# Kernel optimization log

Hardware: AMD Instinct MI355X
Metric: run time of the kernel (lower is better)

## Reference

```python
import jax, jax.numpy as jnp
import numpy as np

B, S1, S2, C = 8, 256, 256, 64
M1, M2 = 32, 32          # n_modes per spatial dim
SCALE = 1.0 / (C * C)    # 1/(in_channels*out_channels)


def setup_inputs() -> dict:
    key = jax.random.key(0)
    ks = jax.random.split(key, 5)
    X = jax.random.normal(ks[0], (B, S1, S2, C), dtype=jnp.float32)
    k0r = SCALE * jax.random.normal(ks[1], (M1, C, C), dtype=jnp.float32)
    k0i = SCALE * jax.random.normal(ks[2], (M1, C, C), dtype=jnp.float32)
    k1r = SCALE * jax.random.normal(ks[3], (M2, C, C), dtype=jnp.float32)
    k1i = SCALE * jax.random.normal(ks[4], (M2, C, C), dtype=jnp.float32)
    return {"X": X, "k0r": k0r, "k0i": k0i, "k1r": k1r, "k1i": k1i}


def reference(X, k0r, k0i, k1r, k1i):
    # Factorized spectral conv: per-spatial-dim rFFT -> truncated-mode
    # complex channel mix -> zero-pad -> irFFT, summed over dims.
    k0 = jax.lax.complex(k0r, k0i)  # (M1, out, in)
    k1 = jax.lax.complex(k1r, k1i)  # (M2, out, in)

    out = jnp.zeros_like(X)

    # --- spatial dim 0 (axis -3) ---
    Xf = jnp.fft.rfft(X, axis=-3, norm="forward")          # (B, S1//2+1, S2, C) complex
    Yt = jnp.einsum("rij,bryj->bryi", k0, Xf[:, :M1])       # truncated-mode channel mix
    Y = jnp.zeros_like(Xf).at[:, :M1].set(Yt)               # zero-pad back to full modes
    out = out + jnp.fft.irfft(Y, n=S1, axis=-3, norm="forward")

    # --- spatial dim 1 (axis -2) ---
    Xf = jnp.fft.rfft(X, axis=-2, norm="forward")           # (B, S1, S2//2+1, C)
    Yt = jnp.einsum("rij,bxrj->bxri", k1, Xf[:, :, :M2])
    Y = jnp.zeros_like(Xf).at[:, :, :M2].set(Yt)
    out = out + jnp.fft.irfft(Y, n=S2, axis=-2, norm="forward")

    return out
```

## Files before the change

kernel.cpp:

```cpp
#include <hip/hip_runtime.h>


namespace {

constexpr int S = 256, C = 64;

typedef _Float16 f16;
typedef _Float16 f16x2 __attribute__((ext_vector_type(2)));
typedef _Float16 f16x4 __attribute__((ext_vector_type(4)));
typedef _Float16 f16x8 __attribute__((ext_vector_type(8)));
typedef float f32x16 __attribute__((ext_vector_type(16)));
typedef unsigned int u32;

constexpr int OFF_FWDF = 0;
constexpr int OFF_INVF = 8192;
constexpr int OFF_A2   = 16384;
constexpr int OFF_YT   = 540672;
constexpr int OFF_XF   = 8929280;
constexpr size_t WS_RMW = (size_t)(OFF_XF + 8388608) * 4;
constexpr size_t WS_PW  = (size_t)(OFF_XF + 16777216) * 4;

constexpr size_t XF_DB = 1048576;
constexpr size_t YT_DB = 1048576;

constexpr int P   = 4624;
constexpr int LDS_BYTES = 8 * P;

__device__ __host__ inline int cadr(int c) { return c * 16 + (c >> 3) * 16; }
__device__ inline int yadr(int r, int c) { return 1152 * r + c * 4 + (c >> 5) * 16; }

__global__ void k_init_all(const float* __restrict__ k0r, const float* __restrict__ k0i,
                           const float* __restrict__ k1r, const float* __restrict__ ki1,
                           float* __restrict__ ws) {
  const int bid = blockIdx.x;
  if (bid < 128) {
    int t = bid * 256 + threadIdx.x;
    f16* fwdF = (f16*)(ws + OFF_FWDF);
    f16* invF = (f16*)(ws + OFF_INVF);
    if (t < 16384) {
      int e = t & 7, lane = (t >> 3) & 63, mtkk = t >> 9;
      int mt = mtkk & 1, kk = mtkk >> 1;
      int mc = mt * 32 + (lane & 31);
      int x = kk * 16 + 8 * (lane >> 5) + e;
      int r = mc >> 1;
      float ang = (float)((r * x) & 255) * (3.14159265358979323846f / 128.0f);
      float v = (mc & 1) ? -sinf(ang) : cosf(ang);
      fwdF[t] = (f16)v;
    } else {
      int t2 = t - 16384;
      int e = t2 & 7, lane = (t2 >> 3) & 63, mtg = (t2 >> 9) & 7, kk = t2 >> 12;
      int u = mtg * 32 + (lane & 31);
      int mcv = kk * 16 + 8 * (lane >> 5) + e;
      int r = mcv >> 1;
      float wgt = (r == 0) ? 1.0f : 2.0f;
      float ang = (float)((r * u) & 255) * (3.14159265358979323846f / 128.0f);
      float v = (mcv & 1) ? -wgt * sinf(ang) : wgt * cosf(ang);
      invF[t2] = (f16)(v * (1.0f / 256.0f));
    }
    return;
  }
  const int db = bid - 128;
  const float* kr = (db < 2048) ? k0r : k1r;
  const float* ki = (db < 2048) ? k0i : ki1;
  f16* A2 = (f16*)(ws + OFF_A2) + ((db < 2048) ? 0 : 524288);
  int t = (db & 2047) * 256 + threadIdx.x;
  int e = t & 7, l = (t >> 3) & 63, kk = (t >> 9) & 7, mt = (t >> 12) & 3, r = t >> 14;
  int m = mt * 32 + (l & 31);
  int kreal = kk * 16 + 8 * (l >> 5) + e;
  int i = m >> 1, imo = m & 1, j = kreal >> 1, imi = kreal & 1;
  int src = (r * 64 + i) * 64 + j;
  float v = (imi == 0) ? ((imo == 0) ? kr[src] : ki[src])
                       : ((imo == 0) ? -ki[src] : kr[src]);
  A2[t] = (f16)v;
}

__launch_bounds__(512, 2)
__global__ void k_dft(const float* __restrict__ X, const float* __restrict__ ws,
                      f16* __restrict__ xfg) {
  __shared__ char sm[LDS_BYTES] __attribute__((aligned(16)));
  const int tid = threadIdx.x;
  const int l = tid & 63, w = tid >> 6;
  const int g2 = l >> 5, l31 = l & 31;
  const int n0 = w * 32;
  const int dim = (int)blockIdx.x >> 9;
  const int local = (int)blockIdx.x & 511;
  const int b = local >> 6;
  const int yt4 = (local & 63) * 4;
  const size_t bbase = (size_t)b * (S * S * C);
  const f16* fwdF = (const f16*)(ws + OFF_FWDF);

  auto gofs = [&](int u, int c) -> size_t {
    if (dim == 0)
      return bbase + (size_t)u * (S * C) + (size_t)(yt4 + (c >> 6)) * C + (c & 63);
    else
      return bbase + (size_t)(yt4 + (c >> 6)) * (S * C) + (size_t)u * C + (c & 63);
  };

  const int ug = w >> 1;
  const int c1 = (w & 1) * 128 + l;
  const int c2 = c1 + 64;

  float r1[8], r2[8];
  auto stage_load = [&](int u0) {
#pragma unroll
    for (int j = 0; j < 8; ++j) r1[j] = X[gofs(u0 + ug * 8 + j, c1)];
#pragma unroll
    for (int j = 0; j < 8; ++j) r2[j] = X[gofs(u0 + ug * 8 + j, c2)];
  };
  auto stage_write = [&](int buf) {
    f16x8 v1, v2;
#pragma unroll
    for (int j = 0; j < 8; ++j) { v1[j] = (f16)r1[j]; v2[j] = (f16)r2[j]; }
    char* base = sm + buf * (4 * P) + ug * P;
    *(f16x8*)(base + cadr(c1)) = v1;
    *(f16x8*)(base + cadr(c2)) = v2;
  };

  f32x16 acc0, acc1;
#pragma unroll
  for (int q = 0; q < 16; ++q) { acc0[q] = 0.f; acc1[q] = 0.f; }

  stage_load(0);
  stage_write(0);
  __syncthreads();

  for (int ch = 0; ch < 8; ++ch) {
    if (ch < 7) stage_load((ch + 1) * 32);
    const char* bbuf = sm + (ch & 1) * (4 * P);
#pragma unroll
    for (int ks = 0; ks < 2; ++ks) {
      const int kk = ch * 2 + ks;
      f16x8 bf = *(const f16x8*)(bbuf + (ks * 2 + g2) * P + cadr(n0 + l31));
      f16x8 a0 = *(const f16x8*)(fwdF + ((size_t)(kk * 2 + 0) * 64 + l) * 8);
      f16x8 a1 = *(const f16x8*)(fwdF + ((size_t)(kk * 2 + 1) * 64 + l) * 8);
      acc0 = __builtin_amdgcn_mfma_f32_32x32x16_f16(a0, bf, acc0, 0, 0, 0);
      acc1 = __builtin_amdgcn_mfma_f32_32x32x16_f16(a1, bf, acc1, 0, 0, 0);
    }
    if (ch < 7) {
      stage_write((ch + 1) & 1);
      __syncthreads();
    }
  }

  {
    f16* xfb = xfg + ((size_t)dim * 8 + b) * XF_DB;
    const int col = n0 + l31;
    const int yl = col >> 6, j = col & 63;
#pragma unroll
    for (int pr = 0; pr < 16; ++pr) {
      const int q = (pr & 7) >> 1, hf = pr & 1;
      const int r = 2 * g2 + 4 * q + hf + (pr >> 3) * 16;
      const int reg = 4 * q + 2 * hf;
      const float v0 = (pr < 8) ? acc0[reg] : acc1[reg];
      const float v1 = (pr < 8) ? acc0[reg + 1] : acc1[reg + 1];
      f16x2 v2 = {(f16)v0, (f16)v1};
      *(f16x2*)(xfb + (size_t)r * 32768 + (size_t)(yt4 + yl) * 128 + 2 * j) = v2;
    }
  }
}

__launch_bounds__(512, 2)
__global__ void k_mix(const float* __restrict__ ws, const f16* __restrict__ xfg,
                      f16* __restrict__ ytg) {
  const int tid = threadIdx.x;
  const int l = tid & 63, w = tid >> 6;
  const int g2 = l >> 5, l31 = l & 31;
  const int dim = (int)blockIdx.x >> 8;
  const int b = ((int)blockIdx.x >> 5) & 7;
  const int r = (int)blockIdx.x & 31;
  const f16* A2f = (const f16*)(ws + OFF_A2) + (size_t)dim * 524288;
  const f16* xfb = xfg + ((size_t)dim * 8 + b) * XF_DB + (size_t)r * 32768;
  f16* ytb = ytg + ((size_t)dim * 8 + b) * YT_DB;
  const int y = w * 32 + l31;
  const size_t ybase = (size_t)(y >> 2) * 16384 + (size_t)(2 * r) * 256 + (y & 3);

  f16x8 bf[8];
#pragma unroll
  for (int kk = 0; kk < 8; ++kk)
    bf[kk] = *(const f16x8*)(xfb + (size_t)y * 128 + kk * 16 + 8 * g2);

#pragma unroll 1
  for (int mt = 0; mt < 4; ++mt) {
    f32x16 acc;
#pragma unroll
    for (int q = 0; q < 16; ++q) acc[q] = 0.f;
#pragma unroll
    for (int kk = 0; kk < 8; ++kk) {
      f16x8 af = *(const f16x8*)(A2f + ((size_t)((r * 4 + mt) * 8 + kk) * 64 + l) * 8);
      acc = __builtin_amdgcn_mfma_f32_32x32x16_f16(af, bf[kk], acc, 0, 0, 0);
    }
#pragma unroll
    for (int t = 0; t < 8; ++t) {
      const int reg = 2 * t;
      const int i = (t & 1) + 4 * (t >> 1) + 2 * g2 + 16 * mt;
      const size_t o = ybase + (size_t)i * 4;
      ytb[o] = (f16)acc[reg];
      ytb[o + 256] = (f16)acc[reg + 1];
    }
  }
}

template <int MODE>
__launch_bounds__(512, 4)
__global__ void k_idft(const float* __restrict__ ws, const f16* __restrict__ ytg,
                       float* __restrict__ out, f16* __restrict__ pw) {
  constexpr int DIM = (MODE == 0 || MODE == 2) ? 0 : 1;
  __shared__ char sm[8 * 4608] __attribute__((aligned(16)));
  const int tid = threadIdx.x;
  const int l = tid & 63, w = tid >> 6;
  const int g2 = l >> 5, l31 = l & 31;
  const int n0 = w * 32;
  const int hh = (int)blockIdx.x >> 9;
  const int local = (int)blockIdx.x & 511;
  const int b = local >> 6;
  const int yt4 = (local & 63) * 4;
  const size_t bbase = (size_t)b * (S * S * C);
  const f16* invF = (const f16*)(ws + OFF_INVF);
  const f16* ytb = ytg + ((size_t)DIM * 8 + b) * YT_DB + (size_t)(yt4 >> 2) * 16384;

#pragma unroll
  for (int p = 0; p < 8; ++p) {
    const int pair = p * 512 + tid;
    const int i = pair & 63, mc = pair >> 6;
    const int kk = mc >> 4, g2s = (mc >> 3) & 1, e = mc & 7;
    f16x4 v = *(const f16x4*)(ytb + (size_t)pair * 4);
    char* slab = sm + (kk * 2 + g2s) * 4608;
#pragma unroll
    for (int yl = 0; yl < 4; ++yl)
      *(f16*)(slab + cadr(yl * 64 + i) + e * 2) = v[yl];
  }
  __syncthreads();

  const int colg = n0 + l31;
  const int yl = colg >> 6, ii = colg & 63;
  f16x8 bf4[4];
#pragma unroll
  for (int kk = 0; kk < 4; ++kk)
    bf4[kk] = *(const f16x8*)(sm + (kk * 2 + g2) * 4608 + cadr(colg));

#pragma unroll 1
  for (int mt = 0; mt < 4; ++mt) {
    f32x16 a4;
#pragma unroll
    for (int q = 0; q < 16; ++q) a4[q] = 0.f;
#pragma unroll
    for (int kk = 0; kk < 4; ++kk) {
      f16x8 A = *(const f16x8*)(invF + ((size_t)(kk * 8 + hh * 4 + mt) * 64 + l) * 8);
      a4 = __builtin_amdgcn_mfma_f32_32x32x16_f16(A, bf4[kk], a4, 0, 0, 0);
    }
    const int u0 = (hh * 4 + mt) * 32;
#pragma unroll
    for (int reg = 0; reg < 16; ++reg) {
      const int u = u0 + (reg & 3) + 8 * (reg >> 2) + 4 * g2;
      size_t g = (DIM == 0)
                     ? bbase + (size_t)u * (S * C) + (size_t)(yt4 + yl) * C + ii
                     : bbase + (size_t)(yt4 + yl) * (S * C) + (size_t)u * C + ii;
      if constexpr (MODE == 0)      out[g] = a4[reg];
      else if constexpr (MODE == 1) out[g] += a4[reg];
      else if constexpr (MODE == 2) pw[g] = (f16)a4[reg];
      else                          out[g] = a4[reg] + (float)pw[g];
    }
  }
}

template <int MODE>
__launch_bounds__(512, 2)
__global__ void k_dim(const float* __restrict__ X, const float* __restrict__ ws,
                      float* __restrict__ out) {
  constexpr int DIM = (MODE == 0) ? 0 : 1;
  __shared__ char sm[LDS_BYTES] __attribute__((aligned(16)));
  const int tid = threadIdx.x;
  const int l = tid & 63, w = tid >> 6;
  const int g2 = l >> 5, l31 = l & 31;
  const int n0 = w * 32;
  const int bid = (DIM == 1) ? (int)(gridDim.x - 1 - blockIdx.x) : (int)blockIdx.x;
  const int b = bid >> 6;
  const int t4 = (bid & 63) * 4;
  const size_t bbase = (size_t)b * (S * S * C);
  const f16* fwdF = (const f16*)(ws + OFF_FWDF);
  const f16* invF = (const f16*)(ws + OFF_INVF);
  const f16* A2 = (const f16*)(ws + OFF_A2) + (DIM == 0 ? 0 : 524288);
  const int colg = n0 + l31;
  const int pp = colg >> 6, jj = colg & 63;

  auto gofs = [&](int u, int c) -> size_t {
    if (DIM == 0)
      return bbase + (size_t)u * (S * C) + (size_t)(t4 + (c >> 6)) * C + (c & 63);
    else
      return bbase + (size_t)(t4 + (c >> 6)) * (S * C) + (size_t)u * C + (c & 63);
  };
  const int ug = w >> 1;
  const int c1 = (w & 1) * 128 + l;
  const int c2 = c1 + 64;
  float r1[8], r2[8];
  auto stage_load = [&](int u0) {
#pragma unroll
    for (int j = 0; j < 8; ++j) r1[j] = X[gofs(u0 + ug * 8 + j, c1)];
#pragma unroll
    for (int j = 0; j < 8; ++j) r2[j] = X[gofs(u0 + ug * 8 + j, c2)];
  };
  auto stage_write = [&](int buf) {
    f16x8 v1, v2;
#pragma unroll
    for (int j = 0; j < 8; ++j) { v1[j] = (f16)r1[j]; v2[j] = (f16)r2[j]; }
    char* base = sm + buf * (4 * P) + ug * P;
    *(f16x8*)(base + cadr(c1)) = v1;
    *(f16x8*)(base + cadr(c2)) = v2;
  };

  f32x16 acc0, acc1;
#pragma unroll
  for (int q = 0; q < 16; ++q) { acc0[q] = 0.f; acc1[q] = 0.f; }
  stage_load(0);
  stage_write(0);
  __syncthreads();
  for (int ch = 0; ch < 8; ++ch) {
    if (ch < 7) stage_load((ch + 1) * 32);
    const char* bbuf = sm + (ch & 1) * (4 * P);
#pragma unroll
    for (int ks = 0; ks < 2; ++ks) {
      const int kk = ch * 2 + ks;
      f16x8 bf = *(const f16x8*)(bbuf + (ks * 2 + g2) * P + cadr(n0 + l31));
      f16x8 a0 = *(const f16x8*)(fwdF + ((size_t)(kk * 2 + 0) * 64 + l) * 8);
      f16x8 a1 = *(const f16x8*)(fwdF + ((size_t)(kk * 2 + 1) * 64 + l) * 8);
      acc0 = __builtin_amdgcn_mfma_f32_32x32x16_f16(a0, bf, acc0, 0, 0, 0);
      acc1 = __builtin_amdgcn_mfma_f32_32x32x16_f16(a1, bf, acc1, 0, 0, 0);
    }
    if (ch < 7) { stage_write((ch + 1) & 1); __syncthreads(); }
  }
  __syncthreads();
  {
    const int col = n0 + l31;
    const int p = col >> 6, j = col & 63;
    const int kk = j >> 3, g2p = (j >> 2) & 1, js = j & 3;
#pragma unroll
    for (int pr = 0; pr < 16; ++pr) {
      const int q = (pr & 7) >> 1, hf = pr & 1;
      const int r = 2 * g2 + 4 * q + hf + (pr >> 3) * 16;
      const int reg = 4 * q + 2 * hf;
      const float v0 = (pr < 8) ? acc0[reg] : acc1[reg];
      const float v1 = (pr < 8) ? acc0[reg + 1] : acc1[reg + 1];
      f16x2 v2 = {(f16)v0, (f16)v1};
      const int W = (r * 16 + kk * 2 + g2p) * 4 + p;
      *(f16x2*)(sm + W * 16 + (W >> 3) * 16 + js * 4) = v2;
    }
  }
  __syncthreads();
  {
    const int colsel = l31 & 3;
#pragma unroll 1
    for (int rq = 0; rq < 4; ++rq) {
      const int r = w * 4 + rq;
      f16x8 bfr[8];
#pragma unroll
      for (int kk = 0; kk < 8; ++kk) {
        const int W = (r * 16 + kk * 2 + g2) * 4 + colsel;
        bfr[kk] = *(const f16x8*)(sm + W * 16 + (W >> 3) * 16);
      }
#pragma unroll 1
      for (int mt = 0; mt < 4; ++mt) {
        f32x16 acc;
#pragma unroll
        for (int q = 0; q < 16; ++q) acc[q] = 0.f;
#pragma unroll
        for (int kk = 0; kk < 8; ++kk) {
          f16x8 af = *(const f16x8*)(A2 + ((size_t)((r * 4 + mt) * 8 + kk) * 64 + l) * 8);
          acc = __builtin_amdgcn_mfma_f32_32x32x16_f16(af, bfr[kk], acc, 0, 0, 0);
        }
        if (l31 < 4) {
#pragma unroll
          for (int t2 = 0; t2 < 8; ++t2) {
            int reg = t2 * 2;
            int rowin = (reg & 3) + 8 * (reg >> 2) + 4 * g2;
            int i = (mt * 32 + rowin) >> 1;
            f16x2 v2 = {(f16)acc[reg], (f16)acc[reg + 1]};
            *(f16x2*)(sm + yadr(r, l31 * 64 + i)) = v2;
          }
        }
      }
    }
  }
  __syncthreads();
  f16x8 bf4[4];
  {
    const int cb = colg * 4 + (colg >> 5) * 16;
#pragma unroll
    for (int kk = 0; kk < 4; ++kk) {
      union { f16x8 h; u32 u[4]; } bb;
      const int r0 = 8 * kk + 4 * g2;
#pragma unroll
      for (int s = 0; s < 4; ++s)
        bb.u[s] = *(const u32*)(sm + 1152 * (r0 + s) + cb);
      bf4[kk] = bb.h;
    }
  }
#pragma unroll 1
  for (int h = 0; h < 2; ++h) {
#pragma unroll 1
    for (int mt = 0; mt < 4; ++mt) {
      f32x16 a4;
#pragma unroll
      for (int q = 0; q < 16; ++q) a4[q] = 0.f;
#pragma unroll
      for (int kk = 0; kk < 4; ++kk) {
        f16x8 A = *(const f16x8*)(invF + ((size_t)(kk * 8 + h * 4 + mt) * 64 + l) * 8);
        a4 = __builtin_amdgcn_mfma_f32_32x32x16_f16(A, bf4[kk], a4, 0, 0, 0);
      }
      const int u0 = (h * 4 + mt) * 32;
#pragma unroll
      for (int reg = 0; reg < 16; ++reg) {
        const int u = u0 + (reg & 3) + 8 * (reg >> 2) + 4 * g2;
        size_t g = (DIM == 0)
                       ? bbase + (size_t)u * (S * C) + (size_t)(t4 + pp) * C + jj
                       : bbase + (size_t)(t4 + pp) * (S * C) + (size_t)u * C + jj;
        if constexpr (MODE == 0) out[g] = a4[reg];
        else                     out[g] += a4[reg];
      }
    }
  }
}

}

extern "C" void kernel_launch(void* const* d_in, const int* in_sizes, int n_in,
                              void* d_out, int out_size, void* d_ws, size_t ws_size,
                              hipStream_t stream) {
  (void)in_sizes; (void)n_in; (void)out_size;
  const float* X   = (const float*)d_in[0];
  const float* k0r = (const float*)d_in[1];
  const float* k0i = (const float*)d_in[2];
  const float* k1r = (const float*)d_in[3];
  const float* k1i = (const float*)d_in[4];
  float* out = (float*)d_out;
  float* ws  = (float*)d_ws;
  f16* ytg = (f16*)(ws + OFF_YT);
  f16* xfg = (f16*)(ws + OFF_XF);
  f16* pw  = (f16*)(ws + OFF_XF);

  k_init_all<<<4224, 256, 0, stream>>>(k0r, k0i, k1r, k1i, ws);
  if (ws_size >= WS_RMW) {
    k_dft<<<1024, 512, 0, stream>>>(X, ws, xfg);
    k_mix<<<512, 512, 0, stream>>>(ws, xfg, ytg);
    if (ws_size >= WS_PW) {
      k_idft<2><<<1024, 512, 0, stream>>>(ws, ytg, out, pw);
      k_idft<3><<<1024, 512, 0, stream>>>(ws, ytg, out, pw);
    } else {
      k_idft<0><<<1024, 512, 0, stream>>>(ws, ytg, out, nullptr);
      k_idft<1><<<1024, 512, 0, stream>>>(ws, ytg, out, nullptr);
    }
  } else {
    k_dim<0><<<512, 512, 0, stream>>>(X, ws, out);
    k_dim<1><<<512, 512, 0, stream>>>(X, ws, out);
  }
}
```

Baseline: 143.6 us.

## Interleave DFT, mix and iDFT stages of the two dims in fused launches

Splits the per-dim pipeline so that the dim-0 mix runs inside the same launch as the dim-1 DFT, and the dim-1 mix runs inside the dim-0 iDFT launch. Block indices are interleaved (every third or fifth block does mix work) so the stages overlap and fill the GPU instead of running as separate, partly idle launches. This needs a separate pw buffer at a new workspace offset, because xfg is still live when the dim-0 iDFT writes pw. That raises the workspace requirement, and the new path runs only when the workspace is large enough. Mixing heterogeneous blocks in one launch may unbalance occupancy, since each launch keeps a single launch bound and LDS size.

```diff
diff --git a/kernel.cpp b/kernel.cpp
--- a/kernel.cpp
+++ b/kernel.cpp
@@ -17,8 +17,10 @@
 constexpr int OFF_A2   = 16384;
 constexpr int OFF_YT   = 540672;
 constexpr int OFF_XF   = 8929280;
-constexpr size_t WS_RMW = (size_t)(OFF_XF + 8388608) * 4;
-constexpr size_t WS_PW  = (size_t)(OFF_XF + 16777216) * 4;
+constexpr int OFF_PW2  = 17317888;
+constexpr size_t WS_RMW  = (size_t)(OFF_XF + 8388608) * 4;
+constexpr size_t WS_PW   = (size_t)(OFF_XF + 16777216) * 4;
+constexpr size_t WS_FULL = (size_t)(OFF_PW2 + 16777216) * 4;
 
 constexpr size_t XF_DB = 1048576;
 constexpr size_t YT_DB = 1048576;
@@ -74,16 +76,14 @@
   A2[t] = (f16)v;
 }
 
-__launch_bounds__(512, 2)
-__global__ void k_dft(const float* __restrict__ X, const float* __restrict__ ws,
-                      f16* __restrict__ xfg) {
-  __shared__ char sm[LDS_BYTES] __attribute__((aligned(16)));
+__device__ inline void dft4_body(int dim, int local, char* sm,
+                                 const float* __restrict__ X,
+                                 const float* __restrict__ ws,
+                                 f16* __restrict__ xfg) {
   const int tid = threadIdx.x;
   const int l = tid & 63, w = tid >> 6;
   const int g2 = l >> 5, l31 = l & 31;
   const int n0 = w * 32;
-  const int dim = (int)blockIdx.x >> 9;
-  const int local = (int)blockIdx.x & 511;
   const int b = local >> 6;
   const int yt4 = (local & 63) * 4;
   const size_t bbase = (size_t)b * (S * S * C);
@@ -159,15 +159,13 @@
   }
 }
 
-__launch_bounds__(512, 2)
-__global__ void k_mix(const float* __restrict__ ws, const f16* __restrict__ xfg,
-                      f16* __restrict__ ytg) {
+__device__ inline void mix_body(int dim, int local, const float* __restrict__ ws,
+                                const f16* __restrict__ xfg, f16* __restrict__ ytg) {
   const int tid = threadIdx.x;
   const int l = tid & 63, w = tid >> 6;
   const int g2 = l >> 5, l31 = l & 31;
-  const int dim = (int)blockIdx.x >> 8;
-  const int b = ((int)blockIdx.x >> 5) & 7;
-  const int r = (int)blockIdx.x & 31;
+  const int b = local >> 5;
+  const int r = local & 31;
   const f16* A2f = (const f16*)(ws + OFF_A2) + (size_t)dim * 524288;
   const f16* xfb = xfg + ((size_t)dim * 8 + b) * XF_DB + (size_t)r * 32768;
   f16* ytb = ytg + ((size_t)dim * 8 + b) * YT_DB;
@@ -201,19 +199,18 @@
 }
 
 template <int MODE>
-__launch_bounds__(512, 4)
-__global__ void k_idft(const float* __restrict__ ws, const f16* __restrict__ ytg,
-                       float* __restrict__ out, f16* __restrict__ pw) {
+__device__ inline void idft_body(int local, char* sm, const float* __restrict__ ws,
+                                 const f16* __restrict__ ytg, float* __restrict__ out,
+                                 f16* __restrict__ pw) {
   constexpr int DIM = (MODE == 0 || MODE == 2) ? 0 : 1;
-  __shared__ char sm[8 * 4608] __attribute__((aligned(16)));
   const int tid = threadIdx.x;
   const int l = tid & 63, w = tid >> 6;
   const int g2 = l >> 5, l31 = l & 31;
   const int n0 = w * 32;
-  const int hh = (int)blockIdx.x >> 9;
-  const int local = (int)blockIdx.x & 511;
-  const int b = local >> 6;
-  const int yt4 = (local & 63) * 4;
+  const int hh = local >> 9;
+  const int loc = local & 511;
+  const int b = loc >> 6;
+  const int yt4 = (loc & 63) * 4;
   const size_t bbase = (size_t)b * (S * S * C);
   const f16* invF = (const f16*)(ws + OFF_INVF);
   const f16* ytb = ytg + ((size_t)DIM * 8 + b) * YT_DB + (size_t)(yt4 >> 2) * 16384;
@@ -261,6 +258,54 @@
       else                          out[g] = a4[reg] + (float)pw[g];
     }
   }
+}
+
+__launch_bounds__(512, 2)
+__global__ void k_dft0(const float* __restrict__ X, const float* __restrict__ ws,
+                       f16* __restrict__ xfg) {
+  __shared__ char sm[LDS_BYTES] __attribute__((aligned(16)));
+  dft4_body(0, (int)blockIdx.x, sm, X, ws, xfg);
+}
+
+__launch_bounds__(512, 2)
+__global__ void k_dftB(const float* __restrict__ X, const float* __restrict__ ws,
+                       f16* __restrict__ xfg) {
+  __shared__ char sm[LDS_BYTES] __attribute__((aligned(16)));
+  dft4_body((int)blockIdx.x >> 9, (int)blockIdx.x & 511, sm, X, ws, xfg);
+}
+
+__launch_bounds__(512, 2)
+__global__ void k_dm(const float* __restrict__ X, const float* __restrict__ ws,
+                     f16* __restrict__ xfg, f16* __restrict__ ytg) {
+  __shared__ char sm[LDS_BYTES] __attribute__((aligned(16)));
+  const int bid = (int)blockIdx.x;
+  if (bid % 3 == 2) mix_body(0, bid / 3, ws, xfg, ytg);
+  else              dft4_body(1, bid - (bid + 1) / 3, sm, X, ws, xfg);
+}
+
+__launch_bounds__(512, 2)
+__global__ void k_mixB(const float* __restrict__ ws, const f16* __restrict__ xfg,
+                       f16* __restrict__ ytg) {
+  mix_body((int)blockIdx.x >> 8, (int)blockIdx.x & 255, ws, xfg, ytg);
+}
+
+template <int MODE>
+__launch_bounds__(512, 4)
+__global__ void k_mi(const float* __restrict__ ws, const f16* __restrict__ xfg,
+                     f16* __restrict__ ytg, float* __restrict__ out,
+                     f16* __restrict__ pw) {
+  __shared__ char sm[8 * 4608] __attribute__((aligned(16)));
+  const int bid = (int)blockIdx.x;
+  if (bid % 5 == 4) mix_body(1, bid / 5, ws, xfg, ytg);
+  else              idft_body<MODE>(bid - (bid + 1) / 5, sm, ws, ytg, out, pw);
+}
+
+template <int MODE>
+__launch_bounds__(512, 4)
+__global__ void k_idft(const float* __restrict__ ws, const f16* __restrict__ ytg,
+                       float* __restrict__ out, f16* __restrict__ pw) {
+  __shared__ char sm[8 * 4608] __attribute__((aligned(16)));
+  idft_body<MODE>((int)blockIdx.x, sm, ws, ytg, out, pw);
 }
 
 template <int MODE>
@@ -435,19 +480,25 @@
   float* ws  = (float*)d_ws;
   f16* ytg = (f16*)(ws + OFF_YT);
   f16* xfg = (f16*)(ws + OFF_XF);
-  f16* pw  = (f16*)(ws + OFF_XF);
 
   k_init_all<<<4224, 256, 0, stream>>>(k0r, k0i, k1r, k1i, ws);
-  if (ws_size >= WS_RMW) {
-    k_dft<<<1024, 512, 0, stream>>>(X, ws, xfg);
-    k_mix<<<512, 512, 0, stream>>>(ws, xfg, ytg);
-    if (ws_size >= WS_PW) {
-      k_idft<2><<<1024, 512, 0, stream>>>(ws, ytg, out, pw);
-      k_idft<3><<<1024, 512, 0, stream>>>(ws, ytg, out, pw);
-    } else {
-      k_idft<0><<<1024, 512, 0, stream>>>(ws, ytg, out, nullptr);
-      k_idft<1><<<1024, 512, 0, stream>>>(ws, ytg, out, nullptr);
-    }
+  if (ws_size >= WS_FULL) {
+    f16* pw = (f16*)(ws + OFF_PW2);
+    k_dft0<<<512, 512, 0, stream>>>(X, ws, xfg);
+    k_dm<<<768, 512, 0, stream>>>(X, ws, xfg, ytg);
+    k_mi<2><<<1280, 512, 0, stream>>>(ws, xfg, ytg, out, pw);
+    k_idft<3><<<1024, 512, 0, stream>>>(ws, ytg, out, pw);
+  } else if (ws_size >= WS_PW) {
+    f16* pw = (f16*)(ws + OFF_XF);
+    k_dftB<<<1024, 512, 0, stream>>>(X, ws, xfg);
+    k_mixB<<<512, 512, 0, stream>>>(ws, xfg, ytg);
+    k_idft<2><<<1024, 512, 0, stream>>>(ws, ytg, out, pw);
+    k_idft<3><<<1024, 512, 0, stream>>>(ws, ytg, out, pw);
+  } else if (ws_size >= WS_RMW) {
+    k_dftB<<<1024, 512, 0, stream>>>(X, ws, xfg);
+    k_mixB<<<512, 512, 0, stream>>>(ws, xfg, ytg);
+    k_idft<0><<<1024, 512, 0, stream>>>(ws, ytg, out, nullptr);
+    k_idft<1><<<1024, 512, 0, stream>>>(ws, ytg, out, nullptr);
   } else {
     k_dim<0><<<512, 512, 0, stream>>>(X, ws, out);
     k_dim<1><<<512, 512, 0, stream>>>(X, ws, out);
```

After: 157.6 us. 9.7% more time.
